# Performance work log

Hardware: AMD Instinct MI355X
Metric: run time of the kernel (lower is better)

The kernel has to match this reference:

```python
import jax, jax.numpy as jnp
import numpy as np

ALPHA = 0.5   # leak rate
GAMMA = 0.01  # input scaling
RHO = 1.0     # target spectral radius
SPARSITY = 0.9  # fraction of zeros in W

T, N_INPUT, N_OUTPUT = 4096, 8192, 2048


def setup_inputs() -> dict:
    key = jax.random.key(0)
    k1, k2, k3, k4 = jax.random.split(key, 4)
    x = jax.random.normal(k1, (T, N_INPUT), dtype=jnp.float32)
    Win = GAMMA * jax.random.normal(k2, (N_INPUT, N_OUTPUT), dtype=jnp.float32)
    mask = (jax.random.uniform(k3, (N_OUTPUT, N_OUTPUT)) < (1.0 - SPARSITY)).astype(jnp.float32)
    W0 = jax.random.normal(k4, (N_OUTPUT, N_OUTPUT), dtype=jnp.float32) * mask
    # spectral-radius normalization (circular-law estimate: radius ~ sqrt(p * N) for
    # density p), standing in for rho * W / max|eig(W)| at init time.
    W = RHO * W0 / jnp.sqrt((1.0 - SPARSITY) * N_OUTPUT)
    return {"x": x, "W": W, "Win": Win}


def reference(x, W, Win):
    # x: [T, nInput]; output: [T, nOutput] (stacked hidden states)
    u_proj = x @ Win  # [T, nOutput], input projection is independent of the recurrence

    def step(v, up):
        # v: [nOutput]  leaky-integrator reservoir update
        v_new = (1.0 - ALPHA) * v + ALPHA * jnp.tanh(v @ W + up)
        return v_new, v_new

    v0 = jnp.zeros((W.shape[0],), dtype=x.dtype)  # ESN starts from zero state
    _, vs = jax.lax.scan(step, v0, u_proj)
    return vs
```

## Files before the change

kernel.cpp:

```cpp
#include <hip/hip_runtime.h>
#include <hip/hip_bf16.h>
#include <math.h>

#define T_STEPS 4096
#define N_IN    8192
#define N_OUT   2048

#define GM_BK 16

__global__ __launch_bounds__(256) void gemm_xwin(const float* __restrict__ X,
                                                 const float* __restrict__ Win,
                                                 float* __restrict__ U) {
    const int K = N_IN, N = N_OUT;
    __shared__ float As[GM_BK][128 + 4];
    __shared__ float Bs[GM_BK][128 + 4];

    const int tid = threadIdx.x;
    const int bm = blockIdx.x;
    const int bn = blockIdx.y;
    const int tx = tid & 15;
    const int ty = tid >> 4;

    float acc[8][8];
#pragma unroll
    for (int i = 0; i < 8; i++)
#pragma unroll
        for (int j = 0; j < 8; j++) acc[i][j] = 0.f;

    const float* Xb = X + (size_t)(bm * 128) * K;
    const float* Wb = Win + bn * 128;

    for (int kt = 0; kt < K; kt += GM_BK) {
#pragma unroll
        for (int q = 0; q < 2; q++) {
            const int r  = (tid >> 2) + q * 64;
            const int c4 = (tid & 3) * 4;
            const float4 a4 = *reinterpret_cast<const float4*>(&Xb[(size_t)r * K + kt + c4]);
            As[c4 + 0][r] = a4.x;
            As[c4 + 1][r] = a4.y;
            As[c4 + 2][r] = a4.z;
            As[c4 + 3][r] = a4.w;
        }
#pragma unroll
        for (int q = 0; q < 2; q++) {
            const int r  = (tid >> 5) + q * 8;
            const int c4 = (tid & 31) * 4;
            *reinterpret_cast<float4*>(&Bs[r][c4]) =
                *reinterpret_cast<const float4*>(&Wb[(size_t)(kt + r) * N + c4]);
        }
        __syncthreads();

#pragma unroll
        for (int k = 0; k < GM_BK; k++) {
            float a[8], b[8];
#pragma unroll
            for (int i = 0; i < 4; i++) {
                a[i]     = As[k][ty * 4 + i];
                a[4 + i] = As[k][64 + ty * 4 + i];
            }
#pragma unroll
            for (int j = 0; j < 4; j++) {
                b[j]     = Bs[k][tx * 4 + j];
                b[4 + j] = Bs[k][64 + tx * 4 + j];
            }
#pragma unroll
            for (int i = 0; i < 8; i++)
#pragma unroll
                for (int j = 0; j < 8; j++)
                    acc[i][j] = fmaf(a[i], b[j], acc[i][j]);
        }
        __syncthreads();
    }

#pragma unroll
    for (int i = 0; i < 8; i++) {
        const int mr = bm * 128 + ((i < 4) ? (ty * 4 + i) : (64 + ty * 4 + (i - 4)));
        float* Crow = U + (size_t)mr * N + bn * 128;
        float4 v0 = make_float4(acc[i][0], acc[i][1], acc[i][2], acc[i][3]);
        float4 v1 = make_float4(acc[i][4], acc[i][5], acc[i][6], acc[i][7]);
        *reinterpret_cast<float4*>(&Crow[tx * 4])      = v0;
        *reinterpret_cast<float4*>(&Crow[64 + tx * 4]) = v1;
    }
}

#define RB   64
#define CPB  32
#define GRP  8
#define CAP  288
#define KMAX (CAP / GRP)

__device__ __forceinline__ float fast_tanh(float x) {
    const float ax = fabsf(x);
    const float e  = __expf(2.0f * ax);
    const float r  = __builtin_amdgcn_rcpf(e + 1.0f);
    const float t  = 1.0f - 2.0f * r;
    return copysignf(t, x);
}

__global__ __launch_bounds__(256, 1) void esn_recur(const float* __restrict__ W,
                                                    float* __restrict__ UO,
                                                    unsigned long long* vslots) {
    __shared__ unsigned long long ent[CPB][CAP];
    __shared__ int   cnts[CPB];
    __shared__ float vsh[2][N_OUT];

    const int tid = threadIdx.x;
    const int b   = blockIdx.x;
    const int c   = tid >> 3;
    const int l   = tid & 7;
    const int j   = b * CPB + c;
    const int lw  = tid & 63;

    int cnt = 0;
    for (int k = 0; k < N_OUT / GRP; k++) {
        const float w = W[(size_t)(l + GRP * k) * N_OUT + j];
        cnt += (w != 0.0f) ? 1 : 0;
    }
    int inc = cnt;
#pragma unroll
    for (int d = 1; d < GRP; d <<= 1) {
        int n = __shfl_up(inc, d, 64);
        if (l >= d) inc += n;
    }
    int pos = inc - cnt;
    if (l == GRP - 1) cnts[c] = inc;
    for (int k = 0; k < N_OUT / GRP; k++) {
        const int i = l + GRP * k;
        const float w = W[(size_t)i * N_OUT + j];
        if (w != 0.0f) {
            if (pos < CAP)
                ent[c][pos] = ((unsigned long long)(unsigned)i << 32) | __float_as_uint(w);
            pos++;
        }
    }
    __syncthreads();
    const int ccnt = min(cnts[c], CAP);

    float wreg[KMAX];
    int   ireg[KMAX];
#pragma unroll
    for (int k = 0; k < KMAX; k++) {
        const int p = l + k * GRP;
        if (p < ccnt) {
            const unsigned long long e = ent[c][p];
            wreg[k] = __uint_as_float((unsigned)e);
            ireg[k] = (int)(e >> 32);
        } else {
            wreg[k] = 0.f;
            ireg[k] = 0;
        }
    }

#pragma unroll
    for (int pass = 0; pass < KMAX; ++pass) {
#pragma unroll
        for (int i = (pass & 1); i + 1 < KMAX; i += 2) {
            const int ka = ((ireg[i]     & 31) - lw) & 31;
            const int kb = ((ireg[i + 1] & 31) - lw) & 31;
            const bool sw = ka > kb;
            const int   ti = sw ? ireg[i] : ireg[i + 1];
            const int   bi = sw ? ireg[i + 1] : ireg[i];
            const float tw = sw ? wreg[i] : wreg[i + 1];
            const float bw = sw ? wreg[i + 1] : wreg[i];
            ireg[i] = bi; ireg[i + 1] = ti;
            wreg[i] = bw; wreg[i + 1] = tw;
        }
    }

#pragma unroll 1
    for (int t = 0; t < T_STEPS; t++) {
        float u = 0.f;
        if (l == 0) u = UO[(size_t)t * N_OUT + j];

        unsigned long long* vin = vslots + (size_t)(t & 1) * N_OUT;
        float* dst = vsh[t & 1];
        unsigned long long uq[8];
#pragma unroll
        for (int q = 0; q < 8; q++)
            uq[q] = __hip_atomic_load(&vin[tid + q * 256], __ATOMIC_RELAXED,
                                      __HIP_MEMORY_SCOPE_AGENT);
        unsigned pend = 0xFFu;
#pragma unroll 1
        while (true) {
            unsigned np = 0;
#pragma unroll
            for (int q = 0; q < 8; q++) {
                if (pend & (1u << q)) {
                    if ((unsigned)(uq[q] >> 32) == (unsigned)t)
                        dst[tid + q * 256] = __uint_as_float((unsigned)uq[q]);
                    else
                        np |= (1u << q);
                }
            }
            pend = np;
            if (!pend) break;
#pragma unroll
            for (int q = 0; q < 8; q++)
                if (pend & (1u << q))
                    uq[q] = __hip_atomic_load(&vin[tid + q * 256], __ATOMIC_RELAXED,
                                              __HIP_MEMORY_SCOPE_AGENT);
        }
        __syncthreads();

        const float* vcur = vsh[t & 1];
        float y0 = 0.f, y1 = 0.f, y2 = 0.f, y3 = 0.f;
#pragma unroll
        for (int k = 0; k < KMAX; k += 4) {
            y0 = fmaf(wreg[k + 0], vcur[ireg[k + 0]], y0);
            y1 = fmaf(wreg[k + 1], vcur[ireg[k + 1]], y1);
            y2 = fmaf(wreg[k + 2], vcur[ireg[k + 2]], y2);
            y3 = fmaf(wreg[k + 3], vcur[ireg[k + 3]], y3);
        }
        float y = (y0 + y1) + (y2 + y3);
#pragma unroll
        for (int d = GRP / 2; d >= 1; d >>= 1) y += __shfl_xor(y, d, 64);

        if (l == 0) {
            const float vnew = 0.5f * vcur[j] + 0.5f * fast_tanh(y + u);
            const unsigned long long slot =
                ((unsigned long long)(unsigned)(t + 1) << 32) | __float_as_uint(vnew);
            __hip_atomic_store(&vslots[(size_t)((t + 1) & 1) * N_OUT + j], slot,
                               __ATOMIC_RELAXED, __HIP_MEMORY_SCOPE_AGENT);
            UO[(size_t)t * N_OUT + j] = vnew;
        }
    }
}

extern "C" void kernel_launch(void* const* d_in, const int* in_sizes, int n_in,
                              void* d_out, int out_size, void* d_ws, size_t ws_size,
                              hipStream_t stream) {
    const float* x   = (const float*)d_in[0];
    const float* W   = (const float*)d_in[1];
    const float* Win = (const float*)d_in[2];
    float* out = (float*)d_out;

    unsigned long long* vslots = (unsigned long long*)d_ws;

    hipMemsetAsync(d_ws, 0, 2 * N_OUT * sizeof(unsigned long long), stream);

    dim3 ggrid(T_STEPS / 128, N_OUT / 128);
    gemm_xwin<<<ggrid, 256, 0, stream>>>(x, Win, out);

    esn_recur<<<RB, 256, 0, stream>>>(W, out, vslots);
}
```

Before: 12.00 ms.

## Fuse input-projection GEMM into recurrence kernel with per-row-tile readiness flags

Merges the x@Win GEMM and the sparse recurrence into one launch. The first 64 blocks run the recurrence while the remaining 512 blocks compute GEMM tiles, and each GEMM tile bumps a per-128-row counter when it finishes. The recurrence spins on that counter every 128 steps, so the sequential scan can start before the whole projection is done. It also rebuilds the sparse W gather in chunks to fit a shared smem buffer, and raises recurrence wave priority. The risks are deadlock if the recurrence blocks are not co-resident with the GEMM blocks, and contention from GEMM blocks sharing CUs with the latency-bound recurrence.

Measured after the change: 14.38 ms. 19.9% more time.

```diff
diff --git a/kernel.cpp b/kernel.cpp
--- a/kernel.cpp
+++ b/kernel.cpp
@@ -6,88 +6,20 @@
 #define N_IN    8192
 #define N_OUT   2048
 
-#define GM_BK 16
-
-__global__ __launch_bounds__(256) void gemm_xwin(const float* __restrict__ X,
-                                                 const float* __restrict__ Win,
-                                                 float* __restrict__ U) {
-    const int K = N_IN, N = N_OUT;
-    __shared__ float As[GM_BK][128 + 4];
-    __shared__ float Bs[GM_BK][128 + 4];
-
-    const int tid = threadIdx.x;
-    const int bm = blockIdx.x;
-    const int bn = blockIdx.y;
-    const int tx = tid & 15;
-    const int ty = tid >> 4;
-
-    float acc[8][8];
-#pragma unroll
-    for (int i = 0; i < 8; i++)
-#pragma unroll
-        for (int j = 0; j < 8; j++) acc[i][j] = 0.f;
-
-    const float* Xb = X + (size_t)(bm * 128) * K;
-    const float* Wb = Win + bn * 128;
-
-    for (int kt = 0; kt < K; kt += GM_BK) {
-#pragma unroll
-        for (int q = 0; q < 2; q++) {
-            const int r  = (tid >> 2) + q * 64;
-            const int c4 = (tid & 3) * 4;
-            const float4 a4 = *reinterpret_cast<const float4*>(&Xb[(size_t)r * K + kt + c4]);
-            As[c4 + 0][r] = a4.x;
-            As[c4 + 1][r] = a4.y;
-            As[c4 + 2][r] = a4.z;
-            As[c4 + 3][r] = a4.w;
-        }
-#pragma unroll
-        for (int q = 0; q < 2; q++) {
-            const int r  = (tid >> 5) + q * 8;
-            const int c4 = (tid & 31) * 4;
-            *reinterpret_cast<float4*>(&Bs[r][c4]) =
-                *reinterpret_cast<const float4*>(&Wb[(size_t)(kt + r) * N + c4]);
-        }
-        __syncthreads();
-
-#pragma unroll
-        for (int k = 0; k < GM_BK; k++) {
-            float a[8], b[8];
-#pragma unroll
-            for (int i = 0; i < 4; i++) {
-                a[i]     = As[k][ty * 4 + i];
-                a[4 + i] = As[k][64 + ty * 4 + i];
-            }
-#pragma unroll
-            for (int j = 0; j < 4; j++) {
-                b[j]     = Bs[k][tx * 4 + j];
-                b[4 + j] = Bs[k][64 + tx * 4 + j];
-            }
-#pragma unroll
-            for (int i = 0; i < 8; i++)
-#pragma unroll
-                for (int j = 0; j < 8; j++)
-                    acc[i][j] = fmaf(a[i], b[j], acc[i][j]);
-        }
-        __syncthreads();
-    }
-
-#pragma unroll
-    for (int i = 0; i < 8; i++) {
-        const int mr = bm * 128 + ((i < 4) ? (ty * 4 + i) : (64 + ty * 4 + (i - 4)));
-        float* Crow = U + (size_t)mr * N + bn * 128;
-        float4 v0 = make_float4(acc[i][0], acc[i][1], acc[i][2], acc[i][3]);
-        float4 v1 = make_float4(acc[i][4], acc[i][5], acc[i][6], acc[i][7]);
-        *reinterpret_cast<float4*>(&Crow[tx * 4])      = v0;
-        *reinterpret_cast<float4*>(&Crow[64 + tx * 4]) = v1;
-    }
-}
-
-#define RB   64
-#define CPB  32
-#define GRP  8
-#define CAP  288
-#define KMAX (CAP / GRP)
+#define RB    64
+#define CPB   32
+#define GRP   8
+#define CAP   288
+#define KMAX  (CAP / GRP)
+#define NMT   32
+#define GEMM_BLOCKS 512
+
+#define SM_ENT   0
+#define SM_CNTS  18432
+#define SM_VSH   (18432 + 64)
+#define SM_BYTES (18432 + 64 + 16384)
+#define SM_GA    0
+#define SM_GB    8448
 
 __device__ __forceinline__ float fast_tanh(float x) {
     const float ax = fabsf(x);
@@ -97,58 +29,150 @@
     return copysignf(t, x);
 }
 
-__global__ __launch_bounds__(256, 1) void esn_recur(const float* __restrict__ W,
-                                                    float* __restrict__ UO,
-                                                    unsigned long long* vslots) {
-    __shared__ unsigned long long ent[CPB][CAP];
-    __shared__ int   cnts[CPB];
-    __shared__ float vsh[2][N_OUT];
-
+__global__ __launch_bounds__(256, 3) void esn_fused(
+        const float* __restrict__ X,
+        const float* __restrict__ W,
+        const float* __restrict__ Win,
+        float* __restrict__ UO,
+        unsigned long long* vslots,
+        int* mcnt) {
+    __shared__ __align__(16) char smem[SM_BYTES];
     const int tid = threadIdx.x;
-    const int b   = blockIdx.x;
-    const int c   = tid >> 3;
-    const int l   = tid & 7;
-    const int j   = b * CPB + c;
-    const int lw  = tid & 63;
-
-    int cnt = 0;
-    for (int k = 0; k < N_OUT / GRP; k++) {
-        const float w = W[(size_t)(l + GRP * k) * N_OUT + j];
-        cnt += (w != 0.0f) ? 1 : 0;
-    }
-    int inc = cnt;
-#pragma unroll
-    for (int d = 1; d < GRP; d <<= 1) {
-        int n = __shfl_up(inc, d, 64);
-        if (l >= d) inc += n;
-    }
-    int pos = inc - cnt;
-    if (l == GRP - 1) cnts[c] = inc;
-    for (int k = 0; k < N_OUT / GRP; k++) {
-        const int i = l + GRP * k;
-        const float w = W[(size_t)i * N_OUT + j];
-        if (w != 0.0f) {
-            if (pos < CAP)
-                ent[c][pos] = ((unsigned long long)(unsigned)i << 32) | __float_as_uint(w);
-            pos++;
-        }
-    }
-    __syncthreads();
-    const int ccnt = min(cnts[c], CAP);
+
+    if (blockIdx.x >= RB) {
+        float (*As)[132] = reinterpret_cast<float(*)[132]>(smem + SM_GA);
+        float (*Bs)[132] = reinterpret_cast<float(*)[132]>(smem + SM_GB);
+        const int gb = (int)blockIdx.x - RB;
+        const int bm = gb >> 4;
+        const int bn = gb & 15;
+        const int K = N_IN, N = N_OUT;
+        const int tx = tid & 15;
+        const int ty = tid >> 4;
+
+        float acc[8][8];
+#pragma unroll
+        for (int i = 0; i < 8; i++)
+#pragma unroll
+            for (int jj = 0; jj < 8; jj++) acc[i][jj] = 0.f;
+
+        const float* Xb = X + (size_t)(bm * 128) * K;
+        const float* Wb = Win + bn * 128;
+
+        for (int kt = 0; kt < K; kt += 16) {
+#pragma unroll
+            for (int q = 0; q < 2; q++) {
+                const int r  = (tid >> 2) + q * 64;
+                const int c4 = (tid & 3) * 4;
+                const float4 a4 = *reinterpret_cast<const float4*>(&Xb[(size_t)r * K + kt + c4]);
+                As[c4 + 0][r] = a4.x;
+                As[c4 + 1][r] = a4.y;
+                As[c4 + 2][r] = a4.z;
+                As[c4 + 3][r] = a4.w;
+            }
+#pragma unroll
+            for (int q = 0; q < 2; q++) {
+                const int r  = (tid >> 5) + q * 8;
+                const int c4 = (tid & 31) * 4;
+                *reinterpret_cast<float4*>(&Bs[r][c4]) =
+                    *reinterpret_cast<const float4*>(&Wb[(size_t)(kt + r) * N + c4]);
+            }
+            __syncthreads();
+
+#pragma unroll
+            for (int k = 0; k < 16; k++) {
+                float a[8], bb[8];
+#pragma unroll
+                for (int i = 0; i < 4; i++) {
+                    a[i]     = As[k][ty * 4 + i];
+                    a[4 + i] = As[k][64 + ty * 4 + i];
+                }
+#pragma unroll
+                for (int jj = 0; jj < 4; jj++) {
+                    bb[jj]     = Bs[k][tx * 4 + jj];
+                    bb[4 + jj] = Bs[k][64 + tx * 4 + jj];
+                }
+#pragma unroll
+                for (int i = 0; i < 8; i++)
+#pragma unroll
+                    for (int jj = 0; jj < 8; jj++)
+                        acc[i][jj] = fmaf(a[i], bb[jj], acc[i][jj]);
+            }
+            __syncthreads();
+        }
+
+#pragma unroll
+        for (int i = 0; i < 8; i++) {
+            const int mr = bm * 128 + ((i < 4) ? (ty * 4 + i) : (64 + ty * 4 + (i - 4)));
+            float* Crow = UO + (size_t)mr * N + bn * 128;
+            float4 v0 = make_float4(acc[i][0], acc[i][1], acc[i][2], acc[i][3]);
+            float4 v1 = make_float4(acc[i][4], acc[i][5], acc[i][6], acc[i][7]);
+            *reinterpret_cast<float4*>(&Crow[tx * 4])      = v0;
+            *reinterpret_cast<float4*>(&Crow[64 + tx * 4]) = v1;
+        }
+        __syncthreads();
+        if (tid == 0)
+            __hip_atomic_fetch_add(&mcnt[bm], 1, __ATOMIC_RELEASE,
+                                   __HIP_MEMORY_SCOPE_AGENT);
+        return;
+    }
+
+    __builtin_amdgcn_s_setprio(1);
+    auto ent  = reinterpret_cast<unsigned long long(*)[CAP]>(smem + SM_ENT);
+    int* cnts = reinterpret_cast<int*>(smem + SM_CNTS);
+    float (*vsh)[N_OUT] = reinterpret_cast<float(*)[N_OUT]>(smem + SM_VSH);
+
+    const int b  = blockIdx.x;
+    const int c  = tid >> 3;
+    const int l  = tid & 7;
+    const int j  = b * CPB + c;
+    const int lw = tid & 63;
 
     float wreg[KMAX];
     int   ireg[KMAX];
-#pragma unroll
-    for (int k = 0; k < KMAX; k++) {
-        const int p = l + k * GRP;
-        if (p < ccnt) {
-            const unsigned long long e = ent[c][p];
-            wreg[k] = __uint_as_float((unsigned)e);
-            ireg[k] = (int)(e >> 32);
-        } else {
-            wreg[k] = 0.f;
-            ireg[k] = 0;
-        }
+#pragma unroll 1
+    for (int chunk = 0; chunk < 4; ++chunk) {
+        const int cs = tid >> 5;
+        const int sl = tid & 31;
+        const int jc = b * CPB + chunk * 8 + cs;
+        int cnt = 0;
+        for (int k = 0; k < N_OUT / 32; ++k)
+            cnt += (W[(size_t)(sl + 32 * k) * N_OUT + jc] != 0.f) ? 1 : 0;
+        int inc = cnt;
+#pragma unroll
+        for (int d = 1; d < 32; d <<= 1) {
+            int n = __shfl_up(inc, d, 64);
+            if (sl >= d) inc += n;
+        }
+        int pos = inc - cnt;
+        if (sl == 31) cnts[cs] = inc;
+        for (int k = 0; k < N_OUT / 32; ++k) {
+            const int i = sl + 32 * k;
+            const float w = W[(size_t)i * N_OUT + jc];
+            if (w != 0.f) {
+                if (pos < CAP)
+                    ent[cs][pos] = ((unsigned long long)(unsigned)i << 32) |
+                                   __float_as_uint(w);
+                pos++;
+            }
+        }
+        __syncthreads();
+        if ((tid >> 6) == chunk) {
+            const int cc   = c & 7;
+            const int ccnt = min(cnts[cc], CAP);
+#pragma unroll
+            for (int k = 0; k < KMAX; ++k) {
+                const int p = l + k * GRP;
+                if (p < ccnt) {
+                    const unsigned long long e = ent[cc][p];
+                    wreg[k] = __uint_as_float((unsigned)e);
+                    ireg[k] = (int)(e >> 32);
+                } else {
+                    wreg[k] = 0.f;
+                    ireg[k] = 0;
+                }
+            }
+        }
+        __syncthreads();
     }
 
 #pragma unroll
@@ -169,9 +193,6 @@
 
 #pragma unroll 1
     for (int t = 0; t < T_STEPS; t++) {
-        float u = 0.f;
-        if (l == 0) u = UO[(size_t)t * N_OUT + j];
-
         unsigned long long* vin = vslots + (size_t)(t & 1) * N_OUT;
         float* dst = vsh[t & 1];
         unsigned long long uq[8];
@@ -202,6 +223,13 @@
         }
         __syncthreads();
 
+        if ((t & 127) == 0) {
+            while (__hip_atomic_load(&mcnt[t >> 7], __ATOMIC_ACQUIRE,
+                                     __HIP_MEMORY_SCOPE_AGENT) < 16) { }
+        }
+        float u = 0.f;
+        if (l == 0) u = UO[(size_t)t * N_OUT + j];
+
         const float* vcur = vsh[t & 1];
         float y0 = 0.f, y1 = 0.f, y2 = 0.f, y3 = 0.f;
 #pragma unroll
@@ -235,11 +263,11 @@
     float* out = (float*)d_out;
 
     unsigned long long* vslots = (unsigned long long*)d_ws;
-
-    hipMemsetAsync(d_ws, 0, 2 * N_OUT * sizeof(unsigned long long), stream);
-
-    dim3 ggrid(T_STEPS / 128, N_OUT / 128);
-    gemm_xwin<<<ggrid, 256, 0, stream>>>(x, Win, out);
-
-    esn_recur<<<RB, 256, 0, stream>>>(W, out, vslots);
+    int* mcnt = (int*)((char*)d_ws + 2 * N_OUT * sizeof(unsigned long long));
+
+    hipMemsetAsync(d_ws, 0,
+                   2 * N_OUT * sizeof(unsigned long long) + NMT * sizeof(int),
+                   stream);
+
+    esn_fused<<<RB + GEMM_BLOCKS, 256, 0, stream>>>(x, W, Win, out, vslots, mcnt);
 }
```
